# Performance work log

Hardware: AMD Instinct MI355X
Metric: run time of the kernel (lower is better)

The kernel has to match this reference:

```python
import jax, jax.numpy as jnp
import numpy as np

D_MODEL = 1024
N_HEADS = 16
D_Q = D_MODEL // N_HEADS
NEG = float(-2**32 + 1)


def setup_inputs() -> dict:
    key = jax.random.key(0)
    ks = jax.random.split(key, 8)
    B, L = 8, 1024
    q = jax.random.normal(ks[0], (B, L, D_MODEL), dtype=jnp.float32)
    k = jax.random.normal(ks[1], (B, L, D_MODEL), dtype=jnp.float32)
    # causal subsequent mask: 1 above the diagonal (positions to be masked)
    subseq_mask = jnp.broadcast_to(
        jnp.triu(jnp.ones((L, L), dtype=jnp.int32), k=1), (B, L, L))
    s = 1.0 / np.sqrt(D_MODEL)
    Wq = jax.random.normal(ks[2], (D_MODEL, D_MODEL), dtype=jnp.float32) * s
    Wk = jax.random.normal(ks[3], (D_MODEL, D_MODEL), dtype=jnp.float32) * s
    Wv = jax.random.normal(ks[4], (D_MODEL, D_MODEL), dtype=jnp.float32) * s
    bq = jax.random.normal(ks[5], (D_MODEL,), dtype=jnp.float32) * 0.01
    bk = jax.random.normal(ks[6], (D_MODEL,), dtype=jnp.float32) * 0.01
    bv = jax.random.normal(ks[7], (D_MODEL,), dtype=jnp.float32) * 0.01
    return {"q": q, "k": k, "subseq_mask": subseq_mask,
            "Wq": Wq, "bq": bq, "Wk": Wk, "bk": bk, "Wv": Wv, "bv": bv}


def reference(q, k, subseq_mask, Wq, bq, Wk, bk, Wv, bv):
    B, Lq, _ = q.shape
    Lk = k.shape[1]
    residual = q
    # projections; heads laid out as (H, B, L, d_q) matching torch permute(2,0,1,3)
    qp = (q @ Wq + bq).reshape(B, Lq, N_HEADS, D_Q).transpose(2, 0, 1, 3)
    kp = (k @ Wk + bk).reshape(B, Lk, N_HEADS, D_Q).transpose(2, 0, 1, 3)
    vp = (k @ Wv + bv).reshape(B, Lk, N_HEADS, D_Q).transpose(2, 0, 1, 3)
    # scaled scores: (H, B, Lq, Lk)
    scores = jnp.einsum('hbqd,hbkd->hbqk', qp, kp) / np.sqrt(D_Q)
    # key mask from PROJECTED k (faithful to source)
    key_masks = jnp.sign(jnp.abs(jnp.sum(kp, -1)))          # (H, B, Lk)
    scores = jnp.where(key_masks[:, :, None, :] == 0, NEG, scores)
    # subsequence (causal) mask, replicated over heads
    scores = jnp.where(subseq_mask[None, :, :, :] == 1, NEG, scores)
    attn = jax.nn.softmax(scores, axis=-1)
    # post-softmax query mask from PROJECTED q (faithful to source)
    query_masks = jnp.sign(jnp.abs(jnp.sum(qp, -1)))        # (H, B, Lq)
    attn = attn * query_masks[:, :, :, None]
    # dropout is identity in eval/reference mode
    out = jnp.einsum('hbqk,hbkd->hbqd', attn, vp)           # (H, B, Lq, d_q)
    out = out.transpose(1, 2, 0, 3).reshape(B, Lq, N_HEADS * D_Q)
    return out + residual
```

## Files before the change

### kernel.cpp

```cpp
#include <hip/hip_runtime.h>
#include <cstdint>
#include <cstddef>

#define DM 1024
#define NH 16
#define DQ 64
#define NB 8
#define LSEQ 1024

typedef __attribute__((ext_vector_type(8))) short short8;
typedef __attribute__((ext_vector_type(4))) float floatx4;

__device__ __forceinline__ unsigned short f2bf(float f) {
  union { float f; unsigned u; } v; v.f = f;
  unsigned r = v.u + 0x7FFFu + ((v.u >> 16) & 1u);
  return (unsigned short)(r >> 16);
}
__device__ __forceinline__ float bf2f(unsigned short u) {
  union { unsigned u; float f; } v; v.u = ((unsigned)u) << 16;
  return v.f;
}

__device__ __forceinline__ void async_load16(const void* g, void* l) {
  __builtin_amdgcn_global_load_lds(
      (const __attribute__((address_space(1))) unsigned int*)g,
      (__attribute__((address_space(3))) unsigned int*)l, 16, 0, 0);
}

__global__ void convert_qk(const float* __restrict__ q, const float* __restrict__ k,
                           unsigned short* __restrict__ qb, unsigned short* __restrict__ kb) {
  size_t i = ((size_t)blockIdx.x * 256 + threadIdx.x) * 4;
  float4 a = *(const float4*)&q[i];
  ushort4 r;
  r.x = f2bf(a.x); r.y = f2bf(a.y); r.z = f2bf(a.z); r.w = f2bf(a.w);
  *(ushort4*)&qb[i] = r;
  float4 b = *(const float4*)&k[i];
  ushort4 s;
  s.x = f2bf(b.x); s.y = f2bf(b.y); s.z = f2bf(b.z); s.w = f2bf(b.w);
  *(ushort4*)&kb[i] = s;
}

__global__ void transpose_w(const float* __restrict__ Wq, const float* __restrict__ Wk,
                            const float* __restrict__ Wv, unsigned short* __restrict__ Wt) {
  int z = blockIdx.z;
  const float* W = (z == 0) ? Wq : (z == 1) ? Wk : Wv;
  __shared__ float tile[32][33];
  int n0 = blockIdx.x * 32, k0 = blockIdx.y * 32;
  int tx = threadIdx.x;
  for (int j = threadIdx.y; j < 32; j += 8)
    tile[j][tx] = W[(size_t)(k0 + j) * DM + n0 + tx];
  __syncthreads();
  unsigned short* o = Wt + (size_t)z * DM * DM;
  for (int j = threadIdx.y; j < 32; j += 8)
    o[(size_t)(n0 + j) * DM + k0 + tx] = f2bf(tile[tx][j]);
}

__global__ __launch_bounds__(256, 4) void gemm_proj(
    const unsigned short* __restrict__ qb, const unsigned short* __restrict__ kb,
    const unsigned short* __restrict__ Wt,
    const float* __restrict__ bq, const float* __restrict__ bk, const float* __restrict__ bv,
    const float* __restrict__ ,
    unsigned short* __restrict__ Pq, unsigned short* __restrict__ Pk,
    unsigned short* __restrict__ Pvt,
    float* __restrict__ qmask, float* __restrict__ kmask) {
  const int z = blockIdx.z;
  const unsigned short* A = (z == 0) ? qb : kb;
  const unsigned short* Bt = Wt + (size_t)z * DM * DM;
  const float* bias = (z == 0) ? bq : (z == 1) ? bk : bv;

  __shared__ unsigned short smem[16384];
  unsigned short* As = smem;
  unsigned short* Bs = smem + 8192;

  const int tid = threadIdx.x;
  const int lane = tid & 63;
  const int wave = tid >> 6;
  const int l16 = lane & 15, quad = lane >> 4;
  const int wm = wave & 1, wn = wave >> 1;
  const int rowBase = blockIdx.x * 128;
  const int colBase = blockIdx.y * 128;

  floatx4 acc[4][4];
  const floatx4 zf = {0.f, 0.f, 0.f, 0.f};
#pragma unroll
  for (int i = 0; i < 4; i++)
#pragma unroll
    for (int j = 0; j < 4; j++) acc[i][j] = zf;

  const int srl = lane >> 3;
  const int sl7 = lane & 7;

  for (int kt = 0; kt < DM; kt += 64) {
#pragma unroll
    for (int cc = wave; cc < 16; cc += 4) {
      const int rl = cc * 8 + srl;
      const int ck = (sl7 ^ (rl & 7)) * 8;
      async_load16(A + (size_t)(rowBase + rl) * DM + kt + ck, &As[cc * 512]);
      async_load16(Bt + (size_t)(colBase + rl) * DM + kt + ck, &Bs[cc * 512]);
    }
    __syncthreads();

#pragma unroll
    for (int c = 0; c < 2; c++) {
      const int chnk = ((c << 2) + quad) ^ (l16 & 7);
      short8 af[4], bfr[4];
#pragma unroll
      for (int i = 0; i < 4; i++)
        af[i] = *(const short8*)&As[(wm * 64 + i * 16 + l16) * 64 + chnk * 8];
#pragma unroll
      for (int j = 0; j < 4; j++)
        bfr[j] = *(const short8*)&Bs[(wn * 64 + j * 16 + l16) * 64 + chnk * 8];
#pragma unroll
      for (int i = 0; i < 4; i++)
#pragma unroll
        for (int j = 0; j < 4; j++)
          acc[i][j] = __builtin_amdgcn_mfma_f32_16x16x32_bf16(af[i], bfr[j], acc[i][j], 0, 0, 0);
    }
    __syncthreads();
  }

#pragma unroll
  for (int j = 0; j < 4; j++) {
    const float bj = bias[colBase + wn * 64 + j * 16 + l16];
#pragma unroll
    for (int i = 0; i < 4; i++)
#pragma unroll
      for (int r = 0; r < 4; r++) acc[i][j][r] += bj;
  }

  if (z < 2) {
    float* mask = (z == 0) ? qmask : kmask;
    const int h = (colBase >> 6) + wn;
#pragma unroll
    for (int i = 0; i < 4; i++)
#pragma unroll
      for (int r = 0; r < 4; r++) {
        float rs = acc[i][0][r] + acc[i][1][r] + acc[i][2][r] + acc[i][3][r];
        rs += __shfl_xor(rs, 1);
        rs += __shfl_xor(rs, 2);
        rs += __shfl_xor(rs, 4);
        rs += __shfl_xor(rs, 8);
        if (l16 == 0) {
          const int row = rowBase + wm * 64 + i * 16 + quad * 4 + r;
          mask[((size_t)((row >> 10) * NH + h)) * LSEQ + (row & 1023)] = (rs != 0.f) ? 1.f : 0.f;
        }
      }
    unsigned short* P = (z == 0) ? Pq : Pk;
#pragma unroll
    for (int j = 0; j < 4; j++) {
      const int col = colBase + wn * 64 + j * 16 + l16;
      const int hh = col >> 6, d = col & 63;
#pragma unroll
      for (int i = 0; i < 4; i++) {
        const int row0 = rowBase + wm * 64 + i * 16 + quad * 4;
#pragma unroll
        for (int r = 0; r < 4; r++) {
          const int rr = row0 + r;
          P[((size_t)((rr >> 10) * NH + hh) * LSEQ + (rr & 1023)) * DQ + d] = f2bf(acc[i][j][r]);
        }
      }
    }
  } else {
    const int b = rowBase >> 10;
    const int l0r = rowBase & 1023;
#pragma unroll
    for (int j = 0; j < 4; j++) {
      __syncthreads();
#pragma unroll
      for (int i = 0; i < 4; i++) {
        ushort4 v;
        v.x = f2bf(acc[i][j][0]); v.y = f2bf(acc[i][j][1]);
        v.z = f2bf(acc[i][j][2]); v.w = f2bf(acc[i][j][3]);
        *(ushort4*)&smem[(wn * 16 + l16) * 136 + wm * 64 + i * 16 + quad * 4] = v;
      }
      __syncthreads();
      const int c = tid >> 3, seg = tid & 7;
      const int col = colBase + (c >> 4) * 64 + j * 16 + (c & 15);
      const int hh = col >> 6, d = col & 63;
      int4 t0 = *(const int4*)&smem[c * 136 + seg * 16];
      int4 t1 = *(const int4*)&smem[c * 136 + seg * 16 + 8];
      const size_t g = ((size_t)((b * NH + hh) * DQ + d)) * LSEQ + l0r + seg * 16;
      *(int4*)&Pvt[g] = t0;
      *(int4*)&Pvt[g + 8] = t1;
    }
  }
}

__global__ __launch_bounds__(256, 4) void attn_kernel(
    const unsigned short* __restrict__ Q, const unsigned short* __restrict__ K,
    const unsigned short* __restrict__ Vt,
    const float* __restrict__ kmask, const float* __restrict__ qmask,
    const float* __restrict__ qin, float* __restrict__ out) {
  const int bh = blockIdx.x;
  const int qblk = 7 - blockIdx.y;
  const int b = bh >> 4, h = bh & 15;
  const size_t base = (size_t)bh * LSEQ * DQ;

  const int tid = threadIdx.x;
  const int lane = tid & 63;
  const int wave = tid >> 6;
  const int l16 = lane & 15, quad = lane >> 4;
  const int qw = qblk * 128 + wave * 32;

  __shared__ unsigned short Ks[2 * 4096];
  __shared__ unsigned short Vs[2 * 4096];
  __shared__ unsigned short Ps[4][2304];

  short8 qf[2][2];
#pragma unroll
  for (int sub = 0; sub < 2; sub++)
#pragma unroll
    for (int c = 0; c < 2; c++) {
      short8 t = *(const short8*)&Q[base + (size_t)(qw + sub * 16 + l16) * DQ + c * 32 + quad * 8];
#pragma unroll
      for (int e = 0; e < 8; e++) t[e] = (short)f2bf(bf2f((unsigned short)t[e]) * 0.125f);
      qf[sub][c] = t;
    }

  const floatx4 zf = {0.f, 0.f, 0.f, 0.f};
  floatx4 o[2][4];
#pragma unroll
  for (int sub = 0; sub < 2; sub++)
#pragma unroll
    for (int jj = 0; jj < 4; jj++) o[sub][jj] = zf;
  float l_p[2][4] = {{0.f, 0.f, 0.f, 0.f}, {0.f, 0.f, 0.f, 0.f}};

  const int swz = (quad ^ (l16 & 7)) * 8;
  const int swz2 = ((quad + 4) ^ (l16 & 7)) * 8;
  const int vswz = (quad ^ (l16 >> 1)) * 8;
  const int vswz2 = ((quad + 4) ^ (l16 >> 1)) * 8;

  const int srl = (lane >> 3);
  const int ktiles = (qblk + 1) * 2;
  const int tmax = 2 * qblk + (wave >> 1);

  {
#pragma unroll
    for (int cc = wave; cc < 8; cc += 4) {
      const int rl = cc * 8 + srl;
      const int ck = ((lane & 7) ^ (rl & 7)) * 8;
      async_load16(&K[base + (size_t)rl * DQ + ck], &Ks[cc * 512]);
      const int cv = ((lane & 7) ^ ((rl >> 1) & 7)) * 8;
      async_load16(&Vt[base + (size_t)rl * LSEQ + cv], &Vs[cc * 512]);
    }
  }
  __syncthreads();

  for (int t = 0; t < ktiles; t++) {
    const int cur = t & 1;
    const int kt = t * 64;
    const bool live = (t <= tmax);

    float km[4];
    if (live) {
#pragma unroll
      for (int ct = 0; ct < 4; ct++) km[ct] = kmask[(size_t)bh * LSEQ + kt + ct * 16 + l16];
    }

    if (t + 1 < ktiles) {
      const int nkt = kt + 64;
      const int nb = (cur ^ 1) * 4096;
#pragma unroll
      for (int cc = wave; cc < 8; cc += 4) {
        const int rl = cc * 8 + srl;
        const int ck = ((lane & 7) ^ (rl & 7)) * 8;
        async_load16(&K[base + (size_t)(nkt + rl) * DQ + ck], &Ks[nb + cc * 512]);
        const int cv = ((lane & 7) ^ ((rl >> 1) & 7)) * 8;
        async_load16(&Vt[base + (size_t)rl * LSEQ + nkt + cv], &Vs[nb + cc * 512]);
      }
    }

    if (live) {
      const unsigned short* Kb = &Ks[cur * 4096];
      const unsigned short* Vb = &Vs[cur * 4096];
      const bool diag = (t == tmax);

#pragma unroll
      for (int sub = 0; sub < 2; sub++) {
        floatx4 s[4];
#pragma unroll
        for (int ct = 0; ct < 4; ct++) {
          const int kr = (ct * 16 + l16) * 64;
          const short8 kf0 = *(const short8*)&Kb[kr + swz];
          const short8 kf1 = *(const short8*)&Kb[kr + swz2];
          floatx4 sv = zf;
          sv = __builtin_amdgcn_mfma_f32_16x16x32_bf16(qf[sub][0], kf0, sv, 0, 0, 0);
          sv = __builtin_amdgcn_mfma_f32_16x16x32_bf16(qf[sub][1], kf1, sv, 0, 0, 0);
          s[ct] = sv;
        }
        const int row0 = qw + sub * 16 + quad * 4;
        unsigned short* pw = &Ps[wave][(sub * 16 + quad * 4) * 72];
        if (diag) {
#pragma unroll
          for (int ct = 0; ct < 4; ct++) {
            const int col = kt + ct * 16 + l16;
#pragma unroll
            for (int r = 0; r < 4; r++) {
              float e = __expf(s[ct][r]) * km[ct];
              e = (col <= row0 + r) ? e : 0.f;
              l_p[sub][r] += e;
              pw[r * 72 + ct * 16 + l16] = f2bf(e);
            }
          }
        } else {
#pragma unroll
          for (int ct = 0; ct < 4; ct++) {
#pragma unroll
            for (int r = 0; r < 4; r++) {
              float e = __expf(s[ct][r]) * km[ct];
              l_p[sub][r] += e;
              pw[r * 72 + ct * 16 + l16] = f2bf(e);
            }
          }
        }
      }
      asm volatile("s_waitcnt lgkmcnt(0)" ::: "memory");

      short8 pf[2][2];
#pragma unroll
      for (int sub = 0; sub < 2; sub++) {
        pf[sub][0] = *(const short8*)&Ps[wave][(sub * 16 + l16) * 72 + quad * 8];
        pf[sub][1] = *(const short8*)&Ps[wave][(sub * 16 + l16) * 72 + 32 + quad * 8];
      }
#pragma unroll
      for (int jj = 0; jj < 4; jj++) {
        const int vr = (jj * 16 + l16) * 64;
        const short8 vf0 = *(const short8*)&Vb[vr + vswz];
        const short8 vf1 = *(const short8*)&Vb[vr + vswz2];
#pragma unroll
        for (int sub = 0; sub < 2; sub++) {
          o[sub][jj] = __builtin_amdgcn_mfma_f32_16x16x32_bf16(pf[sub][0], vf0, o[sub][jj], 0, 0, 0);
          o[sub][jj] = __builtin_amdgcn_mfma_f32_16x16x32_bf16(pf[sub][1], vf1, o[sub][jj], 0, 0, 0);
        }
      }
    }
    __syncthreads();
  }

  const int hd = h * DQ;
#pragma unroll
  for (int sub = 0; sub < 2; sub++)
#pragma unroll
    for (int r = 0; r < 4; r++) {
      float lv = l_p[sub][r];
      lv += __shfl_xor(lv, 1);
      lv += __shfl_xor(lv, 2);
      lv += __shfl_xor(lv, 4);
      lv += __shfl_xor(lv, 8);
      const int row = qw + sub * 16 + quad * 4 + r;
      const float inv = qmask[(size_t)bh * LSEQ + row] / lv;
#pragma unroll
      for (int jj = 0; jj < 4; jj++) {
        const size_t oi = ((size_t)(b * LSEQ + row)) * DM + hd + jj * 16 + l16;
        out[oi] = o[sub][jj][r] * inv + qin[oi];
      }
    }
}

extern "C" void kernel_launch(void* const* d_in, const int* in_sizes, int n_in,
                              void* d_out, int out_size, void* d_ws, size_t ws_size,
                              hipStream_t stream) {
  const float* q = (const float*)d_in[0];
  const float* k = (const float*)d_in[1];
  const float* Wq = (const float*)d_in[3];
  const float* bq = (const float*)d_in[4];
  const float* Wk = (const float*)d_in[5];
  const float* bk = (const float*)d_in[6];
  const float* Wv = (const float*)d_in[7];
  const float* bv = (const float*)d_in[8];
  float* out = (float*)d_out;

  char* w = (char*)d_ws;
  unsigned short* qb = (unsigned short*)(w + 0);
  unsigned short* kb = (unsigned short*)(w + 16777216);
  unsigned short* Wt = (unsigned short*)(w + 33554432);
  unsigned short* Pq = (unsigned short*)(w + 39845888);
  unsigned short* Pk = (unsigned short*)(w + 56623104);
  unsigned short* Pvt = (unsigned short*)(w + 73400320);
  float* qmask = (float*)(w + 90177536);
  float* kmask = (float*)(w + 90701824);

  convert_qk<<<8192, 256, 0, stream>>>(q, k, qb, kb);
  transpose_w<<<dim3(32, 32, 3), dim3(32, 8), 0, stream>>>(Wq, Wk, Wv, Wt);
  gemm_proj<<<dim3(64, 8, 3), 256, 0, stream>>>(qb, kb, Wt, bq, bk, bv, nullptr,
                                                Pq, Pk, Pvt, qmask, kmask);
  attn_kernel<<<dim3(128, 8), 256, 0, stream>>>(Pq, Pk, Pvt, kmask, qmask, q, out);
}
```

Baseline: 252.8 us.

## Merge prep kernels, additive key mask, hoist K fragments, relax attention launch bounds

Combines the bf16 conversion of q/k and the weight transpose into one launch, using an extra grid z-slice for the conversion. The key mask becomes an additive bias (0 or -1e30) folded into the exponent instead of a multiply. In the attention kernel all K fragments are loaded once per tile and the score MFMAs for both sub-rows are issued together, and launch bounds drop from 4 to 3 waves per SIMD to allow more registers. This saves a launch and some LDS reloads but raises register pressure and may lower occupancy.

```diff
diff --git a/kernel.cpp b/kernel.cpp
--- a/kernel.cpp
+++ b/kernel.cpp
@@ -27,22 +27,35 @@
       (__attribute__((address_space(3))) unsigned int*)l, 16, 0, 0);
 }
 
-__global__ void convert_qk(const float* __restrict__ q, const float* __restrict__ k,
-                           unsigned short* __restrict__ qb, unsigned short* __restrict__ kb) {
-  size_t i = ((size_t)blockIdx.x * 256 + threadIdx.x) * 4;
-  float4 a = *(const float4*)&q[i];
-  ushort4 r;
-  r.x = f2bf(a.x); r.y = f2bf(a.y); r.z = f2bf(a.z); r.w = f2bf(a.w);
-  *(ushort4*)&qb[i] = r;
-  float4 b = *(const float4*)&k[i];
-  ushort4 s;
-  s.x = f2bf(b.x); s.y = f2bf(b.y); s.z = f2bf(b.z); s.w = f2bf(b.w);
-  *(ushort4*)&kb[i] = s;
-}
-
-__global__ void transpose_w(const float* __restrict__ Wq, const float* __restrict__ Wk,
-                            const float* __restrict__ Wv, unsigned short* __restrict__ Wt) {
-  int z = blockIdx.z;
+__global__ void prep_kernel(const float* __restrict__ q, const float* __restrict__ k,
+                            const float* __restrict__ Wq, const float* __restrict__ Wk,
+                            const float* __restrict__ Wv,
+                            unsigned short* __restrict__ qb, unsigned short* __restrict__ kb,
+                            unsigned short* __restrict__ Wt) {
+  const int z = blockIdx.z;
+  if (z == 3) {
+    const int t = threadIdx.y * 32 + threadIdx.x;
+    const int bid = blockIdx.y * 32 + blockIdx.x;
+#pragma unroll
+    for (int rep = 0; rep < 4; rep++) {
+      const size_t i = (size_t)rep * 2097152 + ((size_t)bid * 256 + t) * 8;
+      float4 a0 = *(const float4*)&q[i];
+      float4 a1 = *(const float4*)&q[i + 4];
+      ushort4 r0, r1;
+      r0.x = f2bf(a0.x); r0.y = f2bf(a0.y); r0.z = f2bf(a0.z); r0.w = f2bf(a0.w);
+      r1.x = f2bf(a1.x); r1.y = f2bf(a1.y); r1.z = f2bf(a1.z); r1.w = f2bf(a1.w);
+      *(ushort4*)&qb[i] = r0;
+      *(ushort4*)&qb[i + 4] = r1;
+      float4 b0 = *(const float4*)&k[i];
+      float4 b1 = *(const float4*)&k[i + 4];
+      ushort4 s0, s1;
+      s0.x = f2bf(b0.x); s0.y = f2bf(b0.y); s0.z = f2bf(b0.z); s0.w = f2bf(b0.w);
+      s1.x = f2bf(b1.x); s1.y = f2bf(b1.y); s1.z = f2bf(b1.z); s1.w = f2bf(b1.w);
+      *(ushort4*)&kb[i] = s0;
+      *(ushort4*)&kb[i + 4] = s1;
+    }
+    return;
+  }
   const float* W = (z == 0) ? Wq : (z == 1) ? Wk : Wv;
   __shared__ float tile[32][33];
   int n0 = blockIdx.x * 32, k0 = blockIdx.y * 32;
@@ -59,7 +72,6 @@
     const unsigned short* __restrict__ qb, const unsigned short* __restrict__ kb,
     const unsigned short* __restrict__ Wt,
     const float* __restrict__ bq, const float* __restrict__ bk, const float* __restrict__ bv,
-    const float* __restrict__ ,
     unsigned short* __restrict__ Pq, unsigned short* __restrict__ Pk,
     unsigned short* __restrict__ Pvt,
     float* __restrict__ qmask, float* __restrict__ kmask) {
@@ -142,7 +154,9 @@
         rs += __shfl_xor(rs, 8);
         if (l16 == 0) {
           const int row = rowBase + wm * 64 + i * 16 + quad * 4 + r;
-          mask[((size_t)((row >> 10) * NH + h)) * LSEQ + (row & 1023)] = (rs != 0.f) ? 1.f : 0.f;
+          const float mv = (z == 0) ? ((rs != 0.f) ? 1.f : 0.f)
+                                    : ((rs != 0.f) ? 0.f : -1e30f);
+          mask[((size_t)((row >> 10) * NH + h)) * LSEQ + (row & 1023)] = mv;
         }
       }
     unsigned short* P = (z == 0) ? Pq : Pk;
@@ -186,7 +200,7 @@
   }
 }
 
-__global__ __launch_bounds__(256, 4) void attn_kernel(
+__global__ __launch_bounds__(256, 3) void attn_kernel(
     const unsigned short* __restrict__ Q, const unsigned short* __restrict__ K,
     const unsigned short* __restrict__ Vt,
     const float* __restrict__ kmask, const float* __restrict__ qmask,
@@ -275,19 +289,26 @@
       const unsigned short* Vb = &Vs[cur * 4096];
       const bool diag = (t == tmax);
 
+      short8 kf[8];
+#pragma unroll
+      for (int ct = 0; ct < 4; ct++) {
+        const int kr = (ct * 16 + l16) * 64;
+        kf[2 * ct] = *(const short8*)&Kb[kr + swz];
+        kf[2 * ct + 1] = *(const short8*)&Kb[kr + swz2];
+      }
+      floatx4 s[2][4];
+#pragma unroll
+      for (int sub = 0; sub < 2; sub++)
+#pragma unroll
+        for (int ct = 0; ct < 4; ct++) {
+          floatx4 sv = zf;
+          sv = __builtin_amdgcn_mfma_f32_16x16x32_bf16(qf[sub][0], kf[2 * ct], sv, 0, 0, 0);
+          sv = __builtin_amdgcn_mfma_f32_16x16x32_bf16(qf[sub][1], kf[2 * ct + 1], sv, 0, 0, 0);
+          s[sub][ct] = sv;
+        }
+
 #pragma unroll
       for (int sub = 0; sub < 2; sub++) {
-        floatx4 s[4];
-#pragma unroll
-        for (int ct = 0; ct < 4; ct++) {
-          const int kr = (ct * 16 + l16) * 64;
-          const short8 kf0 = *(const short8*)&Kb[kr + swz];
-          const short8 kf1 = *(const short8*)&Kb[kr + swz2];
-          floatx4 sv = zf;
-          sv = __builtin_amdgcn_mfma_f32_16x16x32_bf16(qf[sub][0], kf0, sv, 0, 0, 0);
-          sv = __builtin_amdgcn_mfma_f32_16x16x32_bf16(qf[sub][1], kf1, sv, 0, 0, 0);
-          s[ct] = sv;
-        }
         const int row0 = qw + sub * 16 + quad * 4;
         unsigned short* pw = &Ps[wave][(sub * 16 + quad * 4) * 72];
         if (diag) {
@@ -296,7 +317,7 @@
             const int col = kt + ct * 16 + l16;
 #pragma unroll
             for (int r = 0; r < 4; r++) {
-              float e = __expf(s[ct][r]) * km[ct];
+              float e = __expf(s[sub][ct][r] + km[ct]);
               e = (col <= row0 + r) ? e : 0.f;
               l_p[sub][r] += e;
               pw[r * 72 + ct * 16 + l16] = f2bf(e);
@@ -307,7 +328,7 @@
           for (int ct = 0; ct < 4; ct++) {
 #pragma unroll
             for (int r = 0; r < 4; r++) {
-              float e = __expf(s[ct][r]) * km[ct];
+              float e = __expf(s[sub][ct][r] + km[ct]);
               l_p[sub][r] += e;
               pw[r * 72 + ct * 16 + l16] = f2bf(e);
             }
@@ -380,9 +401,8 @@
   float* qmask = (float*)(w + 90177536);
   float* kmask = (float*)(w + 90701824);
 
-  convert_qk<<<8192, 256, 0, stream>>>(q, k, qb, kb);
-  transpose_w<<<dim3(32, 32, 3), dim3(32, 8), 0, stream>>>(Wq, Wk, Wv, Wt);
-  gemm_proj<<<dim3(64, 8, 3), 256, 0, stream>>>(qb, kb, Wt, bq, bk, bv, nullptr,
+  prep_kernel<<<dim3(32, 32, 4), dim3(32, 8), 0, stream>>>(q, k, Wq, Wk, Wv, qb, kb, Wt);
+  gemm_proj<<<dim3(64, 8, 3), 256, 0, stream>>>(qb, kb, Wt, bq, bk, bv,
                                                 Pq, Pk, Pvt, qmask, kmask);
   attn_kernel<<<dim3(128, 8), 256, 0, stream>>>(Pq, Pk, Pvt, kmask, qmask, q, out);
 }
```

Result: slower. 258.6 us (+2.3%).
